# Performance work log

Hardware: AMD Instinct MI355X
Metric: run time of the kernel (lower is better)

The kernel has to match this reference:

```python
import jax, jax.numpy as jnp
import numpy as np

N_NODES = 100000
N_EDGES = 1600000
IN_FEATS = 128
OUT_FEATS = 48


def setup_inputs() -> dict:
    key = jax.random.key(0)
    ks = jax.random.split(key, 6)
    features = jax.random.normal(ks[0], (N_NODES, IN_FEATS), dtype=jnp.float32)
    # xavier_uniform for W.weight [out, in]
    lim_w = float(np.sqrt(6.0 / (IN_FEATS + OUT_FEATS)))
    W_w = jax.random.uniform(ks[1], (OUT_FEATS, IN_FEATS), dtype=jnp.float32, minval=-lim_w, maxval=lim_w)
    W_b = jnp.zeros((OUT_FEATS,), dtype=jnp.float32)
    # xavier_uniform for attn_w [2*out, 1]
    lim_a = float(np.sqrt(6.0 / (2 * OUT_FEATS + 1)))
    attn_w = jax.random.uniform(ks[2], (2 * OUT_FEATS, 1), dtype=jnp.float32, minval=-lim_a, maxval=lim_a)
    attn_b = jnp.zeros((1,), dtype=jnp.float32)
    src = jax.random.randint(ks[3], (N_EDGES,), 0, N_NODES, dtype=jnp.int32)
    dst = jax.random.randint(ks[4], (N_EDGES,), 0, N_NODES, dtype=jnp.int32)
    return {"features": features, "W_w": W_w, "W_b": W_b,
            "attn_w": attn_w, "attn_b": attn_b, "src": src, "dst": dst}


def reference(features, W_w, W_b, attn_w, attn_b, src, dst):
    n = features.shape[0]
    d = W_w.shape[0]
    # h = W(features)  [N, d]
    h = features @ W_w.T + W_b
    # cat([h[src], h[dst]]) @ attn_w == h[src] @ w_src + h[dst] @ w_dst
    w_src = attn_w[:d, 0]   # [d]
    w_dst = attn_w[d:, 0]   # [d]
    s_src = h @ w_src       # [N]
    s_dst = h @ w_dst       # [N]
    e = s_src[src] + s_dst[dst] + attn_b[0]            # [E]
    e = jax.nn.leaky_relu(e, negative_slope=0.2)
    # edge softmax grouped by destination node
    m = jax.ops.segment_max(e, dst, num_segments=n)     # [N]
    ex = jnp.exp(e - m[dst])                            # [E]
    denom = jax.ops.segment_sum(ex, dst, num_segments=n)  # [N]
    alpha = ex / denom[dst]                             # [E]
    # weighted scatter-sum: out[v] = sum_{(u,v) in E} alpha * h[u]
    msgs = h[src] * alpha[:, None]                      # [E, d]
    out = jax.ops.segment_sum(msgs, dst, num_segments=n)  # [N, d]
    return out
```

## Files before the change

### kernel.cpp

```cpp
#include <hip/hip_runtime.h>

#define NFEAT 128
#define DOUT 48
#define BSH 6
#define BNODES 64
#define PCAP 192
#define BCAP (PCAP * 8)
#define EPT 16
#define NBMAX 1568
#define HSTRIDE 32

typedef __attribute__((ext_vector_type(8))) short bf16x8;
typedef __attribute__((ext_vector_type(4))) float f32x4;

__device__ __forceinline__ float bf_lo(unsigned u) { return __uint_as_float(u << 16); }
__device__ __forceinline__ float bf_hi(unsigned u) { return __uint_as_float(u & 0xFFFF0000u); }
__device__ __forceinline__ unsigned bf_pack(float a, float b) {
    unsigned ua = __float_as_uint(a), ub = __float_as_uint(b);
    ua = (ua + 0x7FFFu + ((ua >> 16) & 1u)) >> 16;
    ub = (ub + 0x7FFFu + ((ub >> 16) & 1u)) & 0xFFFF0000u;
    return ua | ub;
}

__device__ __forceinline__ void split2(float x, short& hi, short& lo) {
    unsigned u = __float_as_uint(x);
    unsigned h = u & 0xFFFF0000u;
    hi = (short)(h >> 16);
    float r = x - __uint_as_float(h);
    unsigned v = __float_as_uint(r);
    lo = (short)((v + 0x7FFFu + ((v >> 16) & 1u)) >> 16);
}

__global__ __launch_bounds__(256) void k_wprep(
    const float* __restrict__ Ww, unsigned* __restrict__ Whl)
{
    int i = blockIdx.x * 256 + threadIdx.x;
    if (i < DOUT * NFEAT) {
        short h, l;
        split2(Ww[i], h, l);
        Whl[i] = (unsigned)(unsigned short)h | ((unsigned)(unsigned short)l << 16);
    }
}

__global__ __launch_bounds__(256) void k_proj(
    const float* __restrict__ feat, const unsigned* __restrict__ Whl,
    const float* __restrict__ Wb, const float* __restrict__ attn_w,
    unsigned* __restrict__ hbf, float* __restrict__ s_src, float* __restrict__ s_dst,
    int n)
{
    __shared__ float hb[128][49];

    int tid  = threadIdx.x;
    int lane = tid & 63;
    int wv   = tid >> 6;
    int g    = lane >> 4;
    int r16  = lane & 15;

    int mbase = blockIdx.x * 128 + wv * 32;
    int na0 = mbase + r16;       if (na0 >= n) na0 = n - 1;
    int na1 = mbase + 16 + r16;  if (na1 >= n) na1 = n - 1;

    const float* fA0 = feat + (size_t)na0 * NFEAT + g * 4;
    const float* fA1 = feat + (size_t)na1 * NFEAT + g * 4;
    const unsigned* wB = Whl + (size_t)r16 * NFEAT + g * 4;

    f32x4 acc[2][3];
#pragma unroll
    for (int mt = 0; mt < 2; ++mt)
#pragma unroll
        for (int nt = 0; nt < 3; ++nt)
            acc[mt][nt] = (f32x4){0.f, 0.f, 0.f, 0.f};

#pragma unroll
    for (int ks = 0; ks < 4; ++ks) {
        f32x4 ra[4];
        uint4 wb[6];
        ra[0] = *(const f32x4*)(fA0 + ks * 32);
        ra[1] = *(const f32x4*)(fA0 + ks * 32 + 16);
        ra[2] = *(const f32x4*)(fA1 + ks * 32);
        ra[3] = *(const f32x4*)(fA1 + ks * 32 + 16);
        wb[0] = *(const uint4*)(wB + ks * 32);
        wb[1] = *(const uint4*)(wB + ks * 32 + 16);
        wb[2] = *(const uint4*)(wB + 16 * NFEAT + ks * 32);
        wb[3] = *(const uint4*)(wB + 16 * NFEAT + ks * 32 + 16);
        wb[4] = *(const uint4*)(wB + 32 * NFEAT + ks * 32);
        wb[5] = *(const uint4*)(wB + 32 * NFEAT + ks * 32 + 16);

        bf16x8 Ah[2], Al[2], Bh[3], Bl[3];
#pragma unroll
        for (int t = 0; t < 2; ++t) {
#pragma unroll
            for (int i = 0; i < 4; ++i) {
                short h, l;
                split2(ra[2 * t][i], h, l);     Ah[t][i] = h;     Al[t][i] = l;
                split2(ra[2 * t + 1][i], h, l); Ah[t][i + 4] = h; Al[t][i + 4] = l;
            }
        }
#pragma unroll
        for (int t = 0; t < 3; ++t) {
            unsigned w0 = wb[2 * t].x, w1 = wb[2 * t].y, w2 = wb[2 * t].z, w3 = wb[2 * t].w;
            unsigned v0 = wb[2 * t + 1].x, v1 = wb[2 * t + 1].y, v2 = wb[2 * t + 1].z, v3 = wb[2 * t + 1].w;
            Bh[t][0] = (short)(w0 & 0xFFFF); Bl[t][0] = (short)(w0 >> 16);
            Bh[t][1] = (short)(w1 & 0xFFFF); Bl[t][1] = (short)(w1 >> 16);
            Bh[t][2] = (short)(w2 & 0xFFFF); Bl[t][2] = (short)(w2 >> 16);
            Bh[t][3] = (short)(w3 & 0xFFFF); Bl[t][3] = (short)(w3 >> 16);
            Bh[t][4] = (short)(v0 & 0xFFFF); Bl[t][4] = (short)(v0 >> 16);
            Bh[t][5] = (short)(v1 & 0xFFFF); Bl[t][5] = (short)(v1 >> 16);
            Bh[t][6] = (short)(v2 & 0xFFFF); Bl[t][6] = (short)(v2 >> 16);
            Bh[t][7] = (short)(v3 & 0xFFFF); Bl[t][7] = (short)(v3 >> 16);
        }
#pragma unroll
        for (int mt = 0; mt < 2; ++mt)
#pragma unroll
            for (int nt = 0; nt < 3; ++nt) {
                acc[mt][nt] = __builtin_amdgcn_mfma_f32_16x16x32_bf16(Ah[mt], Bh[nt], acc[mt][nt], 0, 0, 0);
                acc[mt][nt] = __builtin_amdgcn_mfma_f32_16x16x32_bf16(Al[mt], Bh[nt], acc[mt][nt], 0, 0, 0);
                acc[mt][nt] = __builtin_amdgcn_mfma_f32_16x16x32_bf16(Ah[mt], Bl[nt], acc[mt][nt], 0, 0, 0);
            }
    }

#pragma unroll
    for (int mt = 0; mt < 2; ++mt)
#pragma unroll
        for (int nt = 0; nt < 3; ++nt)
#pragma unroll
            for (int rr = 0; rr < 4; ++rr)
                hb[wv * 32 + mt * 16 + 4 * g + rr][nt * 16 + r16] = acc[mt][nt][rr];
    __syncthreads();

    int node = tid >> 1, part = tid & 1, jb = part * 24;
    int gn = blockIdx.x * 128 + node;
    float v[24];
    float ss = 0.f, sd = 0.f;
#pragma unroll
    for (int j = 0; j < 24; ++j) {
        float x = hb[node][jb + j] + Wb[jb + j];
        v[j] = x;
        ss = fmaf(x, attn_w[jb + j], ss);
        sd = fmaf(x, attn_w[DOUT + jb + j], sd);
    }
    ss += __shfl_xor(ss, 1, 64);
    sd += __shfl_xor(sd, 1, 64);

    if (gn < n) {
#pragma unroll
        for (int q = 0; q < 4; ++q) {
            int sub = part * 4 + q;
            uint4 u;
            u.x = bf_pack(v[6 * q + 0], v[6 * q + 1]);
            u.y = bf_pack(v[6 * q + 2], v[6 * q + 3]);
            u.z = bf_pack(v[6 * q + 4], v[6 * q + 5]);
            u.w = 0;
            *(uint4*)(hbf + (size_t)gn * HSTRIDE + sub * 4) = u;
        }
        if (part == 0) {
            s_src[gn] = ss;
            s_dst[gn] = sd;
        }
    }
}

__global__ __launch_bounds__(256) void k_bin(
    const int4* __restrict__ src4, const int4* __restrict__ dst4,
    const float* __restrict__ s_src, const float* __restrict__ s_dst,
    const float* __restrict__ attn_b,
    int* __restrict__ cursor, int2* __restrict__ ents, int nE, int NB)
{
    __shared__ int hist[NBMAX];
    __shared__ int bas[NBMAX];

    int tid = threadIdx.x;
    int cls = blockIdx.x & 7;
    long long e0 = (long long)blockIdx.x * (256 * EPT) + (long long)tid * EPT;

    for (int t = tid; t < NB; t += 256) hist[t] = 0;
    __syncthreads();

    int s[EPT], d[EPT];
    bool any = (e0 < nE);
#pragma unroll
    for (int q = 0; q < EPT / 4; ++q) {
        int4 sv = any ? src4[e0 / 4 + q] : make_int4(0, 0, 0, 0);
        int4 dv = any ? dst4[e0 / 4 + q] : make_int4(0, 0, 0, 0);
        s[4 * q + 0] = sv.x; s[4 * q + 1] = sv.y; s[4 * q + 2] = sv.z; s[4 * q + 3] = sv.w;
        d[4 * q + 0] = dv.x; d[4 * q + 1] = dv.y; d[4 * q + 2] = dv.z; d[4 * q + 3] = dv.w;
    }

    float vs[EPT], vd[EPT];
#pragma unroll
    for (int u = 0; u < EPT; ++u) vs[u] = s_src[s[u]];
#pragma unroll
    for (int u = 0; u < EPT; ++u) vd[u] = s_dst[d[u]];

    int rank[EPT];
#pragma unroll
    for (int u = 0; u < EPT; ++u)
        rank[u] = (e0 + u < nE) ? atomicAdd(&hist[d[u] >> BSH], 1) : 0;
    __syncthreads();

    for (int t = tid; t < NB; t += 256) {
        int c = hist[t];
        if (c > 0) bas[t] = atomicAdd(cursor + cls * NB + t, c);
    }
    __syncthreads();

    float ab = attn_b[0];
#pragma unroll
    for (int u = 0; u < EPT; ++u) {
        if (e0 + u < nE) {
            float v = vs[u] + vd[u] + ab;
            v = (v > 0.f) ? v : 0.2f * v;
            float x = __expf(v);
            int bkt = d[u] >> BSH;
            int slot = bas[bkt] + rank[u];
            if (slot < PCAP)
                ents[(size_t)bkt * BCAP + cls * PCAP + slot] =
                    make_int2(s[u] | ((d[u] & (BNODES - 1)) << 17), __float_as_int(x));
        }
    }
}

__global__ __launch_bounds__(256) void k_aggb(
    const unsigned* __restrict__ hbf, const int* __restrict__ cursor,
    const int2* __restrict__ ents, float* __restrict__ out, int n, int NB)
{
    __shared__ int2 se[BCAP];
    __shared__ unsigned short sidx[BCAP];
    __shared__ int c1[BNODES], c2[BNODES], lrp[BNODES + 1];
    __shared__ int cp[9];

    int b = blockIdx.x;
    int tid = threadIdx.x;
    const int2* ebase = ents + (size_t)b * BCAP;

    if (tid < BNODES) { c1[tid] = 0; c2[tid] = 0; }
    if (tid < 8) {
        int c = min(cursor[tid * NB + b], PCAP);
        int p = c;
#pragma unroll
        for (int o = 1; o < 8; o <<= 1) {
            int u = __shfl_up(p, o, 64);
            if (tid >= o) p += u;
        }
        cp[tid + 1] = p;
        if (tid == 0) cp[0] = 0;
    }
    __syncthreads();
    int total = cp[8];

#pragma unroll
    for (int c = 0; c < 8; ++c) {
        int s0 = cp[c], s1 = cp[c + 1];
        for (int i = s0 + tid; i < s1; i += 256) {
            int2 v = ebase[c * PCAP + (i - s0)];
            se[i] = v;
            atomicAdd(&c1[((unsigned)v.x) >> 17], 1);
        }
    }
    __syncthreads();

    if (tid < BNODES) {
        int v = c1[tid];
        int p = v;
#pragma unroll
        for (int o = 1; o < 64; o <<= 1) {
            int u = __shfl_up(p, o, 64);
            if (tid >= o) p += u;
        }
        lrp[tid] = p - v;
        if (tid == BNODES - 1) lrp[BNODES] = p;
    }
    __syncthreads();

    for (int i = tid; i < total; i += 256) {
        int dl = ((unsigned)se[i].x) >> 17;
        int pos = lrp[dl] + atomicAdd(&c2[dl], 1);
        sidx[pos] = (unsigned short)i;
    }
    __syncthreads();

    int grp = tid >> 3;
    int sub = tid & 7;
#pragma unroll
    for (int pass = 0; pass < 2; ++pass) {
        int dl = grp + pass * 32;
        int node = (b << BSH) + dl;
        bool live = (node < n);
        int st = lrp[dl];
        int en = live ? lrp[dl + 1] : st;
        float a0 = 0.f, a1 = 0.f, a2 = 0.f, a3 = 0.f, a4 = 0.f, a5 = 0.f, den = 0.f;
        int k = st;
        for (; k + 3 < en; k += 4) {
            int2 e0 = se[sidx[k]];
            int2 e1 = se[sidx[k + 1]];
            int2 e2 = se[sidx[k + 2]];
            int2 e3 = se[sidx[k + 3]];
            uint4 h0 = *(const uint4*)(hbf + (size_t)(e0.x & 0x1FFFF) * HSTRIDE + sub * 4);
            uint4 h1 = *(const uint4*)(hbf + (size_t)(e1.x & 0x1FFFF) * HSTRIDE + sub * 4);
            uint4 h2 = *(const uint4*)(hbf + (size_t)(e2.x & 0x1FFFF) * HSTRIDE + sub * 4);
            uint4 h3 = *(const uint4*)(hbf + (size_t)(e3.x & 0x1FFFF) * HSTRIDE + sub * 4);
            float x0 = __int_as_float(e0.y), x1 = __int_as_float(e1.y);
            float x2 = __int_as_float(e2.y), x3 = __int_as_float(e3.y);
            den += x0; den += x1; den += x2; den += x3;
            a0 = fmaf(x0, bf_lo(h0.x), a0); a1 = fmaf(x0, bf_hi(h0.x), a1);
            a2 = fmaf(x0, bf_lo(h0.y), a2); a3 = fmaf(x0, bf_hi(h0.y), a3);
            a4 = fmaf(x0, bf_lo(h0.z), a4); a5 = fmaf(x0, bf_hi(h0.z), a5);
            a0 = fmaf(x1, bf_lo(h1.x), a0); a1 = fmaf(x1, bf_hi(h1.x), a1);
            a2 = fmaf(x1, bf_lo(h1.y), a2); a3 = fmaf(x1, bf_hi(h1.y), a3);
            a4 = fmaf(x1, bf_lo(h1.z), a4); a5 = fmaf(x1, bf_hi(h1.z), a5);
            a0 = fmaf(x2, bf_lo(h2.x), a0); a1 = fmaf(x2, bf_hi(h2.x), a1);
            a2 = fmaf(x2, bf_lo(h2.y), a2); a3 = fmaf(x2, bf_hi(h2.y), a3);
            a4 = fmaf(x2, bf_lo(h2.z), a4); a5 = fmaf(x2, bf_hi(h2.z), a5);
            a0 = fmaf(x3, bf_lo(h3.x), a0); a1 = fmaf(x3, bf_hi(h3.x), a1);
            a2 = fmaf(x3, bf_lo(h3.y), a2); a3 = fmaf(x3, bf_hi(h3.y), a3);
            a4 = fmaf(x3, bf_lo(h3.z), a4); a5 = fmaf(x3, bf_hi(h3.z), a5);
        }
        for (; k < en; ++k) {
            int2 ed = se[sidx[k]];
            float x = __int_as_float(ed.y);
            den += x;
            uint4 h0 = *(const uint4*)(hbf + (size_t)(ed.x & 0x1FFFF) * HSTRIDE + sub * 4);
            a0 = fmaf(x, bf_lo(h0.x), a0); a1 = fmaf(x, bf_hi(h0.x), a1);
            a2 = fmaf(x, bf_lo(h0.y), a2); a3 = fmaf(x, bf_hi(h0.y), a3);
            a4 = fmaf(x, bf_lo(h0.z), a4); a5 = fmaf(x, bf_hi(h0.z), a5);
        }
        if (live) {
            float inv = (en > st) ? 1.f / den : 0.f;
            float* op = out + (size_t)node * DOUT + sub * 6;
            op[0] = a0 * inv;
            op[1] = a1 * inv;
            op[2] = a2 * inv;
            op[3] = a3 * inv;
            op[4] = a4 * inv;
            op[5] = a5 * inv;
        }
    }
}

extern "C" void kernel_launch(void* const* d_in, const int* in_sizes, int n_in,
                              void* d_out, int out_size, void* d_ws, size_t ws_size,
                              hipStream_t stream) {
    const float* feat   = (const float*)d_in[0];
    const float* Ww     = (const float*)d_in[1];
    const float* Wb     = (const float*)d_in[2];
    const float* attn_w = (const float*)d_in[3];
    const float* attn_b = (const float*)d_in[4];
    const int*   src    = (const int*)d_in[5];
    const int*   dst    = (const int*)d_in[6];

    int n  = in_sizes[0] / NFEAT;
    int nE = in_sizes[5];
    int NB = (n + BNODES - 1) / BNODES;
    int N8 = NB * 8;
    float* out = (float*)d_out;

    unsigned* hbf  = (unsigned*)d_ws;
    float* s_src   = (float*)(hbf + (size_t)n * HSTRIDE);
    float* s_dst   = s_src + n;
    int*   cursor  = (int*)(s_dst + n);
    int2*  ents    = (int2*)(cursor + N8);
    unsigned* Whl  = (unsigned*)(ents + (size_t)NB * BCAP);

    hipMemsetAsync(cursor, 0, (size_t)N8 * sizeof(int), stream);

    k_wprep<<<(DOUT * NFEAT + 255) / 256, 256, 0, stream>>>(Ww, Whl);
    int NBp = (n + 127) / 128;
    k_proj<<<NBp, 256, 0, stream>>>(feat, Whl, Wb, attn_w, hbf, s_src, s_dst, n);
    int nbb = (nE + 256 * EPT - 1) / (256 * EPT);
    k_bin<<<nbb, 256, 0, stream>>>((const int4*)src, (const int4*)dst,
                                   s_src, s_dst, attn_b, cursor, ents, nE, NB);
    k_aggb<<<NB, 256, 0, stream>>>(hbf, cursor, ents, out, n, NB);
}
```

Before: 183.2 us.

## Merge projection and edge binning into one launch, compute edge scores in aggregation

Result: faster. 166.0 us, median of 2 (-9.4%).

```diff
diff --git a/kernel.cpp b/kernel.cpp
--- a/kernel.cpp
+++ b/kernel.cpp
@@ -42,196 +42,189 @@
     }
 }
 
-__global__ __launch_bounds__(256) void k_proj(
+__global__ __launch_bounds__(256) void k_pb(
     const float* __restrict__ feat, const unsigned* __restrict__ Whl,
     const float* __restrict__ Wb, const float* __restrict__ attn_w,
     unsigned* __restrict__ hbf, float* __restrict__ s_src, float* __restrict__ s_dst,
-    int n)
+    const int4* __restrict__ src4, const int4* __restrict__ dst4,
+    int* __restrict__ cursor, unsigned* __restrict__ ents,
+    int n, int nE, int NB, int NBp)
 {
-    __shared__ float hb[128][49];
-
-    int tid  = threadIdx.x;
-    int lane = tid & 63;
-    int wv   = tid >> 6;
-    int g    = lane >> 4;
-    int r16  = lane & 15;
-
-    int mbase = blockIdx.x * 128 + wv * 32;
-    int na0 = mbase + r16;       if (na0 >= n) na0 = n - 1;
-    int na1 = mbase + 16 + r16;  if (na1 >= n) na1 = n - 1;
-
-    const float* fA0 = feat + (size_t)na0 * NFEAT + g * 4;
-    const float* fA1 = feat + (size_t)na1 * NFEAT + g * 4;
-    const unsigned* wB = Whl + (size_t)r16 * NFEAT + g * 4;
-
-    f32x4 acc[2][3];
-#pragma unroll
-    for (int mt = 0; mt < 2; ++mt)
-#pragma unroll
-        for (int nt = 0; nt < 3; ++nt)
-            acc[mt][nt] = (f32x4){0.f, 0.f, 0.f, 0.f};
-
-#pragma unroll
-    for (int ks = 0; ks < 4; ++ks) {
-        f32x4 ra[4];
-        uint4 wb[6];
-        ra[0] = *(const f32x4*)(fA0 + ks * 32);
-        ra[1] = *(const f32x4*)(fA0 + ks * 32 + 16);
-        ra[2] = *(const f32x4*)(fA1 + ks * 32);
-        ra[3] = *(const f32x4*)(fA1 + ks * 32 + 16);
-        wb[0] = *(const uint4*)(wB + ks * 32);
-        wb[1] = *(const uint4*)(wB + ks * 32 + 16);
-        wb[2] = *(const uint4*)(wB + 16 * NFEAT + ks * 32);
-        wb[3] = *(const uint4*)(wB + 16 * NFEAT + ks * 32 + 16);
-        wb[4] = *(const uint4*)(wB + 32 * NFEAT + ks * 32);
-        wb[5] = *(const uint4*)(wB + 32 * NFEAT + ks * 32 + 16);
-
-        bf16x8 Ah[2], Al[2], Bh[3], Bl[3];
-#pragma unroll
-        for (int t = 0; t < 2; ++t) {
-#pragma unroll
-            for (int i = 0; i < 4; ++i) {
-                short h, l;
-                split2(ra[2 * t][i], h, l);     Ah[t][i] = h;     Al[t][i] = l;
-                split2(ra[2 * t + 1][i], h, l); Ah[t][i + 4] = h; Al[t][i + 4] = l;
-            }
-        }
-#pragma unroll
-        for (int t = 0; t < 3; ++t) {
-            unsigned w0 = wb[2 * t].x, w1 = wb[2 * t].y, w2 = wb[2 * t].z, w3 = wb[2 * t].w;
-            unsigned v0 = wb[2 * t + 1].x, v1 = wb[2 * t + 1].y, v2 = wb[2 * t + 1].z, v3 = wb[2 * t + 1].w;
-            Bh[t][0] = (short)(w0 & 0xFFFF); Bl[t][0] = (short)(w0 >> 16);
-            Bh[t][1] = (short)(w1 & 0xFFFF); Bl[t][1] = (short)(w1 >> 16);
-            Bh[t][2] = (short)(w2 & 0xFFFF); Bl[t][2] = (short)(w2 >> 16);
-            Bh[t][3] = (short)(w3 & 0xFFFF); Bl[t][3] = (short)(w3 >> 16);
-            Bh[t][4] = (short)(v0 & 0xFFFF); Bl[t][4] = (short)(v0 >> 16);
-            Bh[t][5] = (short)(v1 & 0xFFFF); Bl[t][5] = (short)(v1 >> 16);
-            Bh[t][6] = (short)(v2 & 0xFFFF); Bl[t][6] = (short)(v2 >> 16);
-            Bh[t][7] = (short)(v3 & 0xFFFF); Bl[t][7] = (short)(v3 >> 16);
-        }
+    __shared__ __align__(16) char smem[128 * 49 * 4];
+
+    int tid = threadIdx.x;
+
+    if (blockIdx.x < NBp) {
+        float (*hb)[49] = (float(*)[49])smem;
+
+        int lane = tid & 63;
+        int wv   = tid >> 6;
+        int g    = lane >> 4;
+        int r16  = lane & 15;
+
+        int mbase = blockIdx.x * 128 + wv * 32;
+        int na0 = mbase + r16;       if (na0 >= n) na0 = n - 1;
+        int na1 = mbase + 16 + r16;  if (na1 >= n) na1 = n - 1;
+
+        const float* fA0 = feat + (size_t)na0 * NFEAT + g * 4;
+        const float* fA1 = feat + (size_t)na1 * NFEAT + g * 4;
+        const unsigned* wB = Whl + (size_t)r16 * NFEAT + g * 4;
+
+        f32x4 acc[2][3];
 #pragma unroll
         for (int mt = 0; mt < 2; ++mt)
 #pragma unroll
-            for (int nt = 0; nt < 3; ++nt) {
-                acc[mt][nt] = __builtin_amdgcn_mfma_f32_16x16x32_bf16(Ah[mt], Bh[nt], acc[mt][nt], 0, 0, 0);
-                acc[mt][nt] = __builtin_amdgcn_mfma_f32_16x16x32_bf16(Al[mt], Bh[nt], acc[mt][nt], 0, 0, 0);
-                acc[mt][nt] = __builtin_amdgcn_mfma_f32_16x16x32_bf16(Ah[mt], Bl[nt], acc[mt][nt], 0, 0, 0);
-            }
-    }
-
-#pragma unroll
-    for (int mt = 0; mt < 2; ++mt)
-#pragma unroll
-        for (int nt = 0; nt < 3; ++nt)
-#pragma unroll
-            for (int rr = 0; rr < 4; ++rr)
-                hb[wv * 32 + mt * 16 + 4 * g + rr][nt * 16 + r16] = acc[mt][nt][rr];
-    __syncthreads();
-
-    int node = tid >> 1, part = tid & 1, jb = part * 24;
-    int gn = blockIdx.x * 128 + node;
-    float v[24];
-    float ss = 0.f, sd = 0.f;
-#pragma unroll
-    for (int j = 0; j < 24; ++j) {
-        float x = hb[node][jb + j] + Wb[jb + j];
-        v[j] = x;
-        ss = fmaf(x, attn_w[jb + j], ss);
-        sd = fmaf(x, attn_w[DOUT + jb + j], sd);
-    }
-    ss += __shfl_xor(ss, 1, 64);
-    sd += __shfl_xor(sd, 1, 64);
-
-    if (gn < n) {
-#pragma unroll
-        for (int q = 0; q < 4; ++q) {
-            int sub = part * 4 + q;
-            uint4 u;
-            u.x = bf_pack(v[6 * q + 0], v[6 * q + 1]);
-            u.y = bf_pack(v[6 * q + 2], v[6 * q + 3]);
-            u.z = bf_pack(v[6 * q + 4], v[6 * q + 5]);
-            u.w = 0;
-            *(uint4*)(hbf + (size_t)gn * HSTRIDE + sub * 4) = u;
-        }
-        if (part == 0) {
-            s_src[gn] = ss;
-            s_dst[gn] = sd;
-        }
-    }
-}
-
-__global__ __launch_bounds__(256) void k_bin(
-    const int4* __restrict__ src4, const int4* __restrict__ dst4,
-    const float* __restrict__ s_src, const float* __restrict__ s_dst,
-    const float* __restrict__ attn_b,
-    int* __restrict__ cursor, int2* __restrict__ ents, int nE, int NB)
-{
-    __shared__ int hist[NBMAX];
-    __shared__ int bas[NBMAX];
-
-    int tid = threadIdx.x;
-    int cls = blockIdx.x & 7;
-    long long e0 = (long long)blockIdx.x * (256 * EPT) + (long long)tid * EPT;
-
-    for (int t = tid; t < NB; t += 256) hist[t] = 0;
-    __syncthreads();
-
-    int s[EPT], d[EPT];
-    bool any = (e0 < nE);
-#pragma unroll
-    for (int q = 0; q < EPT / 4; ++q) {
-        int4 sv = any ? src4[e0 / 4 + q] : make_int4(0, 0, 0, 0);
-        int4 dv = any ? dst4[e0 / 4 + q] : make_int4(0, 0, 0, 0);
-        s[4 * q + 0] = sv.x; s[4 * q + 1] = sv.y; s[4 * q + 2] = sv.z; s[4 * q + 3] = sv.w;
-        d[4 * q + 0] = dv.x; d[4 * q + 1] = dv.y; d[4 * q + 2] = dv.z; d[4 * q + 3] = dv.w;
-    }
-
-    float vs[EPT], vd[EPT];
-#pragma unroll
-    for (int u = 0; u < EPT; ++u) vs[u] = s_src[s[u]];
-#pragma unroll
-    for (int u = 0; u < EPT; ++u) vd[u] = s_dst[d[u]];
-
-    int rank[EPT];
-#pragma unroll
-    for (int u = 0; u < EPT; ++u)
-        rank[u] = (e0 + u < nE) ? atomicAdd(&hist[d[u] >> BSH], 1) : 0;
-    __syncthreads();
-
-    for (int t = tid; t < NB; t += 256) {
-        int c = hist[t];
-        if (c > 0) bas[t] = atomicAdd(cursor + cls * NB + t, c);
-    }
-    __syncthreads();
-
-    float ab = attn_b[0];
-#pragma unroll
-    for (int u = 0; u < EPT; ++u) {
-        if (e0 + u < nE) {
-            float v = vs[u] + vd[u] + ab;
-            v = (v > 0.f) ? v : 0.2f * v;
-            float x = __expf(v);
-            int bkt = d[u] >> BSH;
-            int slot = bas[bkt] + rank[u];
-            if (slot < PCAP)
-                ents[(size_t)bkt * BCAP + cls * PCAP + slot] =
-                    make_int2(s[u] | ((d[u] & (BNODES - 1)) << 17), __float_as_int(x));
+            for (int nt = 0; nt < 3; ++nt)
+                acc[mt][nt] = (f32x4){0.f, 0.f, 0.f, 0.f};
+
+#pragma unroll
+        for (int ks = 0; ks < 4; ++ks) {
+            f32x4 ra[4];
+            uint4 wb[6];
+            ra[0] = *(const f32x4*)(fA0 + ks * 32);
+            ra[1] = *(const f32x4*)(fA0 + ks * 32 + 16);
+            ra[2] = *(const f32x4*)(fA1 + ks * 32);
+            ra[3] = *(const f32x4*)(fA1 + ks * 32 + 16);
+            wb[0] = *(const uint4*)(wB + ks * 32);
+            wb[1] = *(const uint4*)(wB + ks * 32 + 16);
+            wb[2] = *(const uint4*)(wB + 16 * NFEAT + ks * 32);
+            wb[3] = *(const uint4*)(wB + 16 * NFEAT + ks * 32 + 16);
+            wb[4] = *(const uint4*)(wB + 32 * NFEAT + ks * 32);
+            wb[5] = *(const uint4*)(wB + 32 * NFEAT + ks * 32 + 16);
+
+            bf16x8 Ah[2], Al[2], Bh[3], Bl[3];
+#pragma unroll
+            for (int t = 0; t < 2; ++t) {
+#pragma unroll
+                for (int i = 0; i < 4; ++i) {
+                    short h, l;
+                    split2(ra[2 * t][i], h, l);     Ah[t][i] = h;     Al[t][i] = l;
+                    split2(ra[2 * t + 1][i], h, l); Ah[t][i + 4] = h; Al[t][i + 4] = l;
+                }
+            }
+#pragma unroll
+            for (int t = 0; t < 3; ++t) {
+                unsigned w0 = wb[2 * t].x, w1 = wb[2 * t].y, w2 = wb[2 * t].z, w3 = wb[2 * t].w;
+                unsigned v0 = wb[2 * t + 1].x, v1 = wb[2 * t + 1].y, v2 = wb[2 * t + 1].z, v3 = wb[2 * t + 1].w;
+                Bh[t][0] = (short)(w0 & 0xFFFF); Bl[t][0] = (short)(w0 >> 16);
+                Bh[t][1] = (short)(w1 & 0xFFFF); Bl[t][1] = (short)(w1 >> 16);
+                Bh[t][2] = (short)(w2 & 0xFFFF); Bl[t][2] = (short)(w2 >> 16);
+                Bh[t][3] = (short)(w3 & 0xFFFF); Bl[t][3] = (short)(w3 >> 16);
+                Bh[t][4] = (short)(v0 & 0xFFFF); Bl[t][4] = (short)(v0 >> 16);
+                Bh[t][5] = (short)(v1 & 0xFFFF); Bl[t][5] = (short)(v1 >> 16);
+                Bh[t][6] = (short)(v2 & 0xFFFF); Bl[t][6] = (short)(v2 >> 16);
+                Bh[t][7] = (short)(v3 & 0xFFFF); Bl[t][7] = (short)(v3 >> 16);
+            }
+#pragma unroll
+            for (int mt = 0; mt < 2; ++mt)
+#pragma unroll
+                for (int nt = 0; nt < 3; ++nt) {
+                    acc[mt][nt] = __builtin_amdgcn_mfma_f32_16x16x32_bf16(Ah[mt], Bh[nt], acc[mt][nt], 0, 0, 0);
+                    acc[mt][nt] = __builtin_amdgcn_mfma_f32_16x16x32_bf16(Al[mt], Bh[nt], acc[mt][nt], 0, 0, 0);
+                    acc[mt][nt] = __builtin_amdgcn_mfma_f32_16x16x32_bf16(Ah[mt], Bl[nt], acc[mt][nt], 0, 0, 0);
+                }
+        }
+
+#pragma unroll
+        for (int mt = 0; mt < 2; ++mt)
+#pragma unroll
+            for (int nt = 0; nt < 3; ++nt)
+#pragma unroll
+                for (int rr = 0; rr < 4; ++rr)
+                    hb[wv * 32 + mt * 16 + 4 * g + rr][nt * 16 + r16] = acc[mt][nt][rr];
+        __syncthreads();
+
+        int node = tid >> 1, part = tid & 1, jb = part * 24;
+        int gn = blockIdx.x * 128 + node;
+        float v[24];
+        float ss = 0.f, sd = 0.f;
+#pragma unroll
+        for (int j = 0; j < 24; ++j) {
+            float x = hb[node][jb + j] + Wb[jb + j];
+            v[j] = x;
+            ss = fmaf(x, attn_w[jb + j], ss);
+            sd = fmaf(x, attn_w[DOUT + jb + j], sd);
+        }
+        ss += __shfl_xor(ss, 1, 64);
+        sd += __shfl_xor(sd, 1, 64);
+
+        if (gn < n) {
+#pragma unroll
+            for (int q = 0; q < 4; ++q) {
+                int sub = part * 4 + q;
+                uint4 u;
+                u.x = bf_pack(v[6 * q + 0], v[6 * q + 1]);
+                u.y = bf_pack(v[6 * q + 2], v[6 * q + 3]);
+                u.z = bf_pack(v[6 * q + 4], v[6 * q + 5]);
+                u.w = 0;
+                *(uint4*)(hbf + (size_t)gn * HSTRIDE + sub * 4) = u;
+            }
+            if (part == 0) {
+                s_src[gn] = ss;
+                s_dst[gn] = sd;
+            }
+        }
+    } else {
+        int* hist = (int*)smem;
+        int* bas  = hist + NBMAX;
+
+        int bb  = blockIdx.x - NBp;
+        int cls = bb & 7;
+        long long e0 = (long long)bb * (256 * EPT) + (long long)tid * EPT;
+
+        for (int t = tid; t < NB; t += 256) hist[t] = 0;
+        __syncthreads();
+
+        int s[EPT], d[EPT];
+        bool any = (e0 < nE);
+#pragma unroll
+        for (int q = 0; q < EPT / 4; ++q) {
+            int4 sv = any ? src4[e0 / 4 + q] : make_int4(0, 0, 0, 0);
+            int4 dv = any ? dst4[e0 / 4 + q] : make_int4(0, 0, 0, 0);
+            s[4 * q + 0] = sv.x; s[4 * q + 1] = sv.y; s[4 * q + 2] = sv.z; s[4 * q + 3] = sv.w;
+            d[4 * q + 0] = dv.x; d[4 * q + 1] = dv.y; d[4 * q + 2] = dv.z; d[4 * q + 3] = dv.w;
+        }
+
+        int rank[EPT];
+#pragma unroll
+        for (int u = 0; u < EPT; ++u)
+            rank[u] = (e0 + u < nE) ? atomicAdd(&hist[d[u] >> BSH], 1) : 0;
+        __syncthreads();
+
+        for (int t = tid; t < NB; t += 256) {
+            int c = hist[t];
+            if (c > 0) bas[t] = atomicAdd(cursor + cls * NB + t, c);
+        }
+        __syncthreads();
+
+#pragma unroll
+        for (int u = 0; u < EPT; ++u) {
+            if (e0 + u < nE) {
+                int bkt = d[u] >> BSH;
+                int slot = bas[bkt] + rank[u];
+                if (slot < PCAP)
+                    ents[(size_t)bkt * BCAP + cls * PCAP + slot] =
+                        (unsigned)s[u] | ((unsigned)(d[u] & (BNODES - 1)) << 17);
+            }
         }
     }
 }
 
 __global__ __launch_bounds__(256) void k_aggb(
     const unsigned* __restrict__ hbf, const int* __restrict__ cursor,
-    const int2* __restrict__ ents, float* __restrict__ out, int n, int NB)
+    const unsigned* __restrict__ ents, const float* __restrict__ s_src,
+    const float* __restrict__ s_dst, const float* __restrict__ attn_b,
+    float* __restrict__ out, int n, int NB)
 {
-    __shared__ int2 se[BCAP];
+    __shared__ unsigned se[BCAP];
     __shared__ unsigned short sidx[BCAP];
     __shared__ int c1[BNODES], c2[BNODES], lrp[BNODES + 1];
     __shared__ int cp[9];
 
     int b = blockIdx.x;
     int tid = threadIdx.x;
-    const int2* ebase = ents + (size_t)b * BCAP;
+    const unsigned* ebase = ents + (size_t)b * BCAP;
+    float ab = attn_b[0];
 
     if (tid < BNODES) { c1[tid] = 0; c2[tid] = 0; }
     if (tid < 8) {
@@ -252,9 +245,9 @@
     for (int c = 0; c < 8; ++c) {
         int s0 = cp[c], s1 = cp[c + 1];
         for (int i = s0 + tid; i < s1; i += 256) {
-            int2 v = ebase[c * PCAP + (i - s0)];
+            unsigned v = ebase[c * PCAP + (i - s0)];
             se[i] = v;
-            atomicAdd(&c1[((unsigned)v.x) >> 17], 1);
+            atomicAdd(&c1[v >> 17], 1);
         }
     }
     __syncthreads();
@@ -273,7 +266,7 @@
     __syncthreads();
 
     for (int i = tid; i < total; i += 256) {
-        int dl = ((unsigned)se[i].x) >> 17;
+        int dl = (int)(se[i] >> 17);
         int pos = lrp[dl] + atomicAdd(&c2[dl], 1);
         sidx[pos] = (unsigned short)i;
     }
@@ -286,21 +279,25 @@
         int dl = grp + pass * 32;
         int node = (b << BSH) + dl;
         bool live = (node < n);
+        float sdn = live ? (s_dst[node] + ab) : 0.f;
         int st = lrp[dl];
         int en = live ? lrp[dl + 1] : st;
         float a0 = 0.f, a1 = 0.f, a2 = 0.f, a3 = 0.f, a4 = 0.f, a5 = 0.f, den = 0.f;
         int k = st;
         for (; k + 3 < en; k += 4) {
-            int2 e0 = se[sidx[k]];
-            int2 e1 = se[sidx[k + 1]];
-            int2 e2 = se[sidx[k + 2]];
-            int2 e3 = se[sidx[k + 3]];
-            uint4 h0 = *(const uint4*)(hbf + (size_t)(e0.x & 0x1FFFF) * HSTRIDE + sub * 4);
-            uint4 h1 = *(const uint4*)(hbf + (size_t)(e1.x & 0x1FFFF) * HSTRIDE + sub * 4);
-            uint4 h2 = *(const uint4*)(hbf + (size_t)(e2.x & 0x1FFFF) * HSTRIDE + sub * 4);
-            uint4 h3 = *(const uint4*)(hbf + (size_t)(e3.x & 0x1FFFF) * HSTRIDE + sub * 4);
-            float x0 = __int_as_float(e0.y), x1 = __int_as_float(e1.y);
-            float x2 = __int_as_float(e2.y), x3 = __int_as_float(e3.y);
+            int i0 = se[sidx[k]]     & 0x1FFFF;
+            int i1 = se[sidx[k + 1]] & 0x1FFFF;
+            int i2 = se[sidx[k + 2]] & 0x1FFFF;
+            int i3 = se[sidx[k + 3]] & 0x1FFFF;
+            float w0 = s_src[i0], w1 = s_src[i1], w2 = s_src[i2], w3 = s_src[i3];
+            uint4 h0 = *(const uint4*)(hbf + (size_t)i0 * HSTRIDE + sub * 4);
+            uint4 h1 = *(const uint4*)(hbf + (size_t)i1 * HSTRIDE + sub * 4);
+            uint4 h2 = *(const uint4*)(hbf + (size_t)i2 * HSTRIDE + sub * 4);
+            uint4 h3 = *(const uint4*)(hbf + (size_t)i3 * HSTRIDE + sub * 4);
+            float v0 = w0 + sdn; v0 = (v0 > 0.f) ? v0 : 0.2f * v0; float x0 = __expf(v0);
+            float v1 = w1 + sdn; v1 = (v1 > 0.f) ? v1 : 0.2f * v1; float x1 = __expf(v1);
+            float v2 = w2 + sdn; v2 = (v2 > 0.f) ? v2 : 0.2f * v2; float x2 = __expf(v2);
+            float v3 = w3 + sdn; v3 = (v3 > 0.f) ? v3 : 0.2f * v3; float x3 = __expf(v3);
             den += x0; den += x1; den += x2; den += x3;
             a0 = fmaf(x0, bf_lo(h0.x), a0); a1 = fmaf(x0, bf_hi(h0.x), a1);
             a2 = fmaf(x0, bf_lo(h0.y), a2); a3 = fmaf(x0, bf_hi(h0.y), a3);
@@ -316,13 +313,14 @@
             a4 = fmaf(x3, bf_lo(h3.z), a4); a5 = fmaf(x3, bf_hi(h3.z), a5);
         }
         for (; k < en; ++k) {
-            int2 ed = se[sidx[k]];
-            float x = __int_as_float(ed.y);
-            den += x;
-            uint4 h0 = *(const uint4*)(hbf + (size_t)(ed.x & 0x1FFFF) * HSTRIDE + sub * 4);
-            a0 = fmaf(x, bf_lo(h0.x), a0); a1 = fmaf(x, bf_hi(h0.x), a1);
-            a2 = fmaf(x, bf_lo(h0.y), a2); a3 = fmaf(x, bf_hi(h0.y), a3);
-            a4 = fmaf(x, bf_lo(h0.z), a4); a5 = fmaf(x, bf_hi(h0.z), a5);
+            int i0 = se[sidx[k]] & 0x1FFFF;
+            float w0 = s_src[i0];
+            uint4 h0 = *(const uint4*)(hbf + (size_t)i0 * HSTRIDE + sub * 4);
+            float v0 = w0 + sdn; v0 = (v0 > 0.f) ? v0 : 0.2f * v0; float x0 = __expf(v0);
+            den += x0;
+            a0 = fmaf(x0, bf_lo(h0.x), a0); a1 = fmaf(x0, bf_hi(h0.x), a1);
+            a2 = fmaf(x0, bf_lo(h0.y), a2); a3 = fmaf(x0, bf_hi(h0.y), a3);
+            a4 = fmaf(x0, bf_lo(h0.z), a4); a5 = fmaf(x0, bf_hi(h0.z), a5);
         }
         if (live) {
             float inv = (en > st) ? 1.f / den : 0.f;
@@ -358,16 +356,16 @@
     float* s_src   = (float*)(hbf + (size_t)n * HSTRIDE);
     float* s_dst   = s_src + n;
     int*   cursor  = (int*)(s_dst + n);
-    int2*  ents    = (int2*)(cursor + N8);
-    unsigned* Whl  = (unsigned*)(ents + (size_t)NB * BCAP);
+    unsigned* ents = (unsigned*)(cursor + N8);
+    unsigned* Whl  = ents + (size_t)NB * BCAP;
 
     hipMemsetAsync(cursor, 0, (size_t)N8 * sizeof(int), stream);
 
     k_wprep<<<(DOUT * NFEAT + 255) / 256, 256, 0, stream>>>(Ww, Whl);
     int NBp = (n + 127) / 128;
-    k_proj<<<NBp, 256, 0, stream>>>(feat, Whl, Wb, attn_w, hbf, s_src, s_dst, n);
     int nbb = (nE + 256 * EPT - 1) / (256 * EPT);
-    k_bin<<<nbb, 256, 0, stream>>>((const int4*)src, (const int4*)dst,
-                                   s_src, s_dst, attn_b, cursor, ents, nE, NB);
-    k_aggb<<<NB, 256, 0, stream>>>(hbf, cursor, ents, out, n, NB);
-}
+    k_pb<<<NBp + nbb, 256, 0, stream>>>(feat, Whl, Wb, attn_w, hbf, s_src, s_dst,
+                                        (const int4*)src, (const int4*)dst,
+                                        cursor, ents, n, nE, NB, NBp);
+    k_aggb<<<NB, 256, 0, stream>>>(hbf, cursor, ents, s_src, s_dst, attn_b, out, n, NB);
+}
```
